# Kernel optimization log

Measured on AMD Instinct MI355X. Metric: run time of the kernel, lower is better.

## Reference

```python
import jax, jax.numpy as jnp
import numpy as np

N = 100_000      # nodes
E = 1_600_000    # edges (avg degree 16)
C_IN, C_H, C_OUT = 32, 64, 64
G = 64           # graphs in batch


def setup_inputs() -> dict:
    key = jax.random.key(0)
    ks = jax.random.split(key, 10)
    x = jax.random.normal(ks[0], (N, C_IN), jnp.float32)
    edge_index = jax.random.randint(ks[1], (2, E), 0, N, dtype=jnp.int64)
    edge_weight = jax.random.uniform(ks[2], (E,), jnp.float32)
    batch = jnp.sort(jax.random.randint(ks[3], (N,), 0, G, dtype=jnp.int64))
    def lin(k, fan_in, fan_out):
        return jax.random.normal(k, (fan_in, fan_out), jnp.float32) / np.float32(np.sqrt(fan_in))
    W1 = lin(ks[4], C_IN, C_H)
    W2 = lin(ks[5], C_H, C_H)
    W3 = lin(ks[6], C_H, C_OUT)
    b1 = jnp.zeros((C_H,), jnp.float32)
    b2 = jnp.zeros((C_H,), jnp.float32)
    b3 = jnp.zeros((C_OUT,), jnp.float32)
    return {"x": x, "edge_weight": edge_weight, "W1": W1, "b1": b1,
            "W2": W2, "b2": b2, "W3": W3, "b3": b3,
            "edge_index": edge_index, "batch": batch}


def _gcn_norm(edge_index, edge_weight, n):
    # PyG GCNConv default: add self-loops (weight 1), symmetric D^-1/2 A D^-1/2 norm.
    loop = jnp.arange(n, dtype=edge_index.dtype)
    src = jnp.concatenate([edge_index[0], loop])
    dst = jnp.concatenate([edge_index[1], loop])
    ew = jnp.concatenate([edge_weight, jnp.ones((n,), edge_weight.dtype)])
    deg = jax.ops.segment_sum(ew, dst, num_segments=n)
    dis = jnp.where(deg > 0, jax.lax.rsqrt(deg), jnp.float32(0))
    norm = dis[src] * ew * dis[dst]
    return src, dst, norm


def _gcn_layer(h, W, b, src, dst, norm, n):
    h = h @ W                                 # [N, out]
    msg = h[src] * norm[:, None]              # gather + scale  [E+N, out]
    agg = jax.ops.segment_sum(msg, dst, num_segments=n)
    return agg + b


def reference(x, edge_weight, W1, b1, W2, b2, W3, b3, edge_index, batch):
    n = x.shape[0]
    src, dst, norm = _gcn_norm(edge_index, edge_weight, n)  # shared across layers
    h = jax.nn.silu(_gcn_layer(x, W1, b1, src, dst, norm, n))
    # Dropout(0.1) is identity in eval mode
    h = jax.nn.silu(_gcn_layer(h, W2, b2, src, dst, norm, n))
    h = jax.nn.silu(_gcn_layer(h, W3, b3, src, dst, norm, n))
    # global_mean_pool over graphs
    sums = jax.ops.segment_sum(h, batch, num_segments=G)
    counts = jax.ops.segment_sum(jnp.ones((n,), h.dtype), batch, num_segments=G)
    return sums / jnp.maximum(counts, 1)[:, None]
```

## Files before the change

kernel.cpp:

```cpp
#include <hip/hip_runtime.h>
#include <hip/hip_fp16.h>
#include <math.h>


#define NB   256
#define PBLK 1024
#define FIXP_SCALE 1048576.0f
#define FIXP_MASK  ((1ULL << 40) - 1)

__device__ __forceinline__ int lower_bound_i(const int* __restrict__ a, int n, int v) {
    int lo = 0, hi = n;
    while (lo < hi) {
        int m = (lo + hi) >> 1;
        if (a[m] < v) lo = m + 1; else hi = m;
    }
    return lo;
}

__global__ __launch_bounds__(256) void k_bhist(const int* __restrict__ dst,
                                               int* __restrict__ hcnt, int e) {
    __shared__ int hist[NB];
    int tid = threadIdx.x, blk = blockIdx.x;
    hist[tid] = 0;
    __syncthreads();
    int chunk = (e + PBLK - 1) / PBLK;
    int lo = blk * chunk, hi = min(e, lo + chunk);
    for (int i = lo + tid; i < hi; i += 256)
        atomicAdd(&hist[dst[i] >> 9], 1);
    __syncthreads();
    hcnt[tid * PBLK + blk] = hist[tid];
}

__global__ __launch_bounds__(256) void k_bscan(int* __restrict__ hcnt,
                                               int* __restrict__ btot) {
    __shared__ int s[256];
    int b = blockIdx.x, tid = threadIdx.x;
    int* row = hcnt + b * PBLK;
    int a0 = row[4 * tid], a1 = row[4 * tid + 1], a2 = row[4 * tid + 2], a3 = row[4 * tid + 3];
    int tsum = a0 + a1 + a2 + a3;
    s[tid] = tsum;
    __syncthreads();
    for (int off = 1; off < 256; off <<= 1) {
        int t = (tid >= off) ? s[tid - off] : 0;
        __syncthreads();
        s[tid] += t;
        __syncthreads();
    }
    int ex = s[tid] - tsum;
    row[4 * tid] = ex;
    row[4 * tid + 1] = ex + a0;
    row[4 * tid + 2] = ex + a0 + a1;
    row[4 * tid + 3] = ex + a0 + a1 + a2;
    if (tid == 255) btot[b] = s[255];
}

__global__ __launch_bounds__(256) void k_bbase(const int* __restrict__ btot,
                                               int* __restrict__ bbase,
                                               int* __restrict__ rowptr, int n, int e) {
    __shared__ int s[256];
    int tid = threadIdx.x;
    int v = btot[tid];
    s[tid] = v;
    __syncthreads();
    for (int off = 1; off < 256; off <<= 1) {
        int t = (tid >= off) ? s[tid - off] : 0;
        __syncthreads();
        s[tid] += t;
        __syncthreads();
    }
    bbase[tid] = s[tid] - v;
    if (tid == 255) bbase[NB] = s[255];
    if (tid == 0) rowptr[n] = e;
}

__global__ __launch_bounds__(256) void k_bpart(const int* __restrict__ src,
                                               const int* __restrict__ dst,
                                               const float* __restrict__ ew,
                                               const int* __restrict__ hcnt,
                                               const int* __restrict__ bbase,
                                               int2* __restrict__ bedge, int e) {
    __shared__ int cur[NB];
    int tid = threadIdx.x, blk = blockIdx.x;
    cur[tid] = bbase[tid] + hcnt[tid * PBLK + blk];
    __syncthreads();
    int chunk = (e + PBLK - 1) / PBLK;
    int lo = blk * chunk, hi = min(e, lo + chunk);
    for (int i = lo + tid; i < hi; i += 256) {
        int d = dst[i];
        int pos = atomicAdd(&cur[d >> 9], 1);
        bedge[pos] = make_int2(src[i] | ((d & 511) << 17), __float_as_int(ew[i]));
    }
}

__global__ __launch_bounds__(256) void k_bucket(const int2* __restrict__ bedge,
                                                const int* __restrict__ bbase,
                                                float* __restrict__ dis,
                                                int* __restrict__ rowptr,
                                                int2* __restrict__ em, int n) {
    __shared__ unsigned long long pk[512];
    __shared__ int cnt[512];
    __shared__ int scn[512];
    __shared__ float sdis[512];
    __shared__ int cur[512];
    int b = blockIdx.x, tid = threadIdx.x;
    int e0 = bbase[b], e1 = bbase[b + 1];
    pk[tid] = 0ULL; pk[tid + 256] = 0ULL;
    __syncthreads();
    for (int i = e0 + tid; i < e1; i += 256) {
        int2 v = bedge[i];
        int dlo = (v.x >> 17) & 511;
        unsigned long long p =
            (1ULL << 40) | (unsigned long long)(__int_as_float(v.y) * FIXP_SCALE);
        atomicAdd(&pk[dlo], p);
    }
    __syncthreads();
#pragma unroll
    for (int k = 0; k < 2; ++k) {
        int i = tid + k * 256;
        unsigned long long v = pk[i];
        int c = (int)(v >> 40);
        cnt[i] = c; scn[i] = c;
        sdis[i] = rsqrtf(1.0f + (float)(v & FIXP_MASK) * (1.0f / FIXP_SCALE));
    }
    __syncthreads();
    for (int off = 1; off < 512; off <<= 1) {
        int i0 = tid, i1 = tid + 256;
        int v0 = (i0 >= off) ? scn[i0 - off] : 0;
        int v1 = (i1 >= off) ? scn[i1 - off] : 0;
        __syncthreads();
        scn[i0] += v0; scn[i1] += v1;
        __syncthreads();
    }
#pragma unroll
    for (int k = 0; k < 2; ++k) {
        int i = tid + k * 256;
        int rb = e0 + scn[i] - cnt[i];
        cur[i] = rb;
        int node = (b << 9) + i;
        if (node < n) { rowptr[node] = rb; dis[node] = sdis[i]; }
    }
    __syncthreads();
    for (int i = e0 + tid; i < e1; i += 256) {
        int2 v = bedge[i];
        int dlo = (v.x >> 17) & 511;
        int pos = atomicAdd(&cur[dlo], 1);
        float w = __int_as_float(v.y) * sdis[dlo];
        em[pos] = make_int2(v.x & 0x1FFFF, __float_as_int(w));
    }
}

__global__ void k_scale(const float* __restrict__ x, const float* __restrict__ dis,
                        __half* __restrict__ hs, int total) {
    int idx = blockIdx.x * blockDim.x + threadIdx.x;
    if (idx < total) hs[idx] = __float2half(x[idx] * dis[idx >> 5]);
}

__device__ __forceinline__ float2 cvt_pair(unsigned int u) {
    __half2 h2 = *(__half2*)&u;
    return __half22float2(h2);
}

__global__ __launch_bounds__(256, 4) void k_agg32(const __half* __restrict__ hs,
                                                  const int2* __restrict__ em,
                                                  const int* __restrict__ rowptr,
                                                  const float* __restrict__ dis,
                                                  __half* __restrict__ y0, int n) {
    __shared__ __align__(8) int2 sme[4][128];
    int lane = threadIdx.x & 63, wv = threadIdx.x >> 6;
    int c = lane & 15, quarter = lane >> 4;
    const unsigned int* h32 = (const unsigned int*)hs;
    int wid = (blockIdx.x * blockDim.x + threadIdx.x) >> 6;
    int n0 = wid * 8;
    if (n0 >= n) return;
    int cnt = min(8, n - n0);
    int rp = 0;
    if (lane <= cnt) rp = rowptr[n0 + lane];
    int hiw = __shfl(rp, cnt, 64);
    int wlo = 0, whi = 0;
    for (int k = 0; k < cnt; ++k) {
        int node = n0 + k;
        int lo = __shfl(rp, k, 64), hi = __shfl(rp, k + 1, 64);
        float2 acc = make_float2(0.0f, 0.0f);
        if (quarter == 0) {
            float di = dis[node];
            float2 hv = cvt_pair(h32[(unsigned)(node * 16 + c)]);
            acc.x = di * hv.x; acc.y = di * hv.y;
        }
        int idx = lo;
        while (idx < hi) {
            if (idx >= whi) {
                int i0 = idx + lane;
                if (i0 < hiw) sme[wv][lane] = em[i0];
                if (idx + 64 < hiw) {
                    int i1 = i0 + 64;
                    if (i1 < hiw) sme[wv][lane + 64] = em[i1];
                }
                wlo = idx; whi = idx + 128;
            }
            int base = idx - wlo;
            int take = min(hi, whi) - idx;
            for (int g = 0; g < take; g += 16) {
                int2 ev[4]; unsigned int hv[4]; int pr[4];
#pragma unroll
                for (int t = 0; t < 4; ++t) {
                    int p = g + 4 * t + quarter;
                    pr[t] = p < take;
                    int pc = pr[t] ? p : 0;
                    ev[t] = sme[wv][base + pc];
                }
#pragma unroll
                for (int t = 0; t < 4; ++t)
                    hv[t] = h32[(unsigned)(ev[t].x * 16 + c)];
#pragma unroll
                for (int t = 0; t < 4; ++t) {
                    float ww = pr[t] ? __int_as_float(ev[t].y) : 0.0f;
                    float2 hf = cvt_pair(hv[t]);
                    acc.x = fmaf(ww, hf.x, acc.x);
                    acc.y = fmaf(ww, hf.y, acc.y);
                }
            }
            idx += take;
        }
        acc.x += __shfl_down(acc.x, 32, 64);
        acc.y += __shfl_down(acc.y, 32, 64);
        acc.x += __shfl_down(acc.x, 16, 64);
        acc.y += __shfl_down(acc.y, 16, 64);
        if (quarter == 0)
            ((__half2*)y0)[(size_t)node * 16 + c] =
                __float22half2_rn(make_float2(acc.x, acc.y));
    }
}

__global__ __launch_bounds__(256, 2) void k_mm32act(const __half* __restrict__ y0,
                                                    const float* __restrict__ W,
                                                    const float* __restrict__ bias,
                                                    const float* __restrict__ dis,
                                                    __half* __restrict__ out, int n) {
    __shared__ __align__(16) float sw[32 * 64 + 64];
#pragma unroll
    for (int i = 0; i < 8; ++i)
        sw[threadIdx.x + 256 * i] = W[threadIdx.x + 256 * i];
    if (threadIdx.x < 64) sw[2048 + threadIdx.x] = bias[threadIdx.x];
    __syncthreads();
    int node = blockIdx.x * 256 + threadIdx.x;
    if (node >= n) return;
    uint4 yp[4];
    const uint4* yrow = (const uint4*)(y0 + (size_t)node * 32);
#pragma unroll
    for (int i = 0; i < 4; ++i) yp[i] = yrow[i];
    const unsigned int* ypk = (const unsigned int*)yp;
    float o[64];
#pragma unroll
    for (int j = 0; j < 64; ++j) o[j] = sw[2048 + j];
#pragma unroll
    for (int k2 = 0; k2 < 16; ++k2) {
        float2 yk = cvt_pair(ypk[k2]);
        const float4* r0 = (const float4*)&sw[(2 * k2) * 64];
        const float4* r1 = (const float4*)&sw[(2 * k2 + 1) * 64];
#pragma unroll
        for (int j4 = 0; j4 < 16; ++j4) {
            float4 w0 = r0[j4];
            float4 w1 = r1[j4];
            o[4 * j4 + 0] = fmaf(yk.y, w1.x, fmaf(yk.x, w0.x, o[4 * j4 + 0]));
            o[4 * j4 + 1] = fmaf(yk.y, w1.y, fmaf(yk.x, w0.y, o[4 * j4 + 1]));
            o[4 * j4 + 2] = fmaf(yk.y, w1.z, fmaf(yk.x, w0.z, o[4 * j4 + 2]));
            o[4 * j4 + 3] = fmaf(yk.y, w1.w, fmaf(yk.x, w0.w, o[4 * j4 + 3]));
        }
    }
    float dsc = dis[node];
    __half2* orow = (__half2*)(out + (size_t)node * 64);
#pragma unroll
    for (int j2 = 0; j2 < 32; ++j2) {
        float ox = o[2 * j2], oy = o[2 * j2 + 1];
        ox = ox / (1.0f + __expf(-ox)) * dsc;
        oy = oy / (1.0f + __expf(-oy)) * dsc;
        orow[j2] = __float22half2_rn(make_float2(ox, oy));
    }
}

__global__ __launch_bounds__(256, 2) void k_mm64(const __half* __restrict__ y,
                                                 const float* __restrict__ W,
                                                 __half* __restrict__ z, int n) {
    __shared__ __align__(16) float sw[64 * 64];
#pragma unroll
    for (int i = 0; i < 16; ++i)
        sw[threadIdx.x + 256 * i] = W[threadIdx.x + 256 * i];
    __syncthreads();
    int node = blockIdx.x * 256 + threadIdx.x;
    if (node >= n) return;
    uint4 yp[8];
    const uint4* yrow = (const uint4*)(y + (size_t)node * 64);
#pragma unroll
    for (int i = 0; i < 8; ++i) yp[i] = yrow[i];
    const unsigned int* ypk = (const unsigned int*)yp;
    float o[64];
#pragma unroll
    for (int j = 0; j < 64; ++j) o[j] = 0.0f;
#pragma unroll
    for (int k2 = 0; k2 < 32; ++k2) {
        float2 yk = cvt_pair(ypk[k2]);
        const float4* r0 = (const float4*)&sw[(2 * k2) * 64];
        const float4* r1 = (const float4*)&sw[(2 * k2 + 1) * 64];
#pragma unroll
        for (int j4 = 0; j4 < 16; ++j4) {
            float4 w0 = r0[j4];
            float4 w1 = r1[j4];
            o[4 * j4 + 0] = fmaf(yk.y, w1.x, fmaf(yk.x, w0.x, o[4 * j4 + 0]));
            o[4 * j4 + 1] = fmaf(yk.y, w1.y, fmaf(yk.x, w0.y, o[4 * j4 + 1]));
            o[4 * j4 + 2] = fmaf(yk.y, w1.z, fmaf(yk.x, w0.z, o[4 * j4 + 2]));
            o[4 * j4 + 3] = fmaf(yk.y, w1.w, fmaf(yk.x, w0.w, o[4 * j4 + 3]));
        }
    }
    __half2* zrow = (__half2*)(z + (size_t)node * 64);
#pragma unroll
    for (int j2 = 0; j2 < 32; ++j2)
        zrow[j2] = __float22half2_rn(make_float2(o[2 * j2], o[2 * j2 + 1]));
}

template <bool SCALE, typename OUT>
__global__ __launch_bounds__(256, 4) void k_agg64(const __half* __restrict__ z,
                                                  const int2* __restrict__ em,
                                                  const int* __restrict__ rowptr,
                                                  const float* __restrict__ dis,
                                                  const float* __restrict__ bias,
                                                  OUT* __restrict__ out, int n) {
    __shared__ __align__(8) int2 sme[4][128];
    int lane = threadIdx.x & 63, wv = threadIdx.x >> 6;
    int c = lane & 31, half = lane >> 5;
    const unsigned int* h32 = (const unsigned int*)z;
    float2 bv2 = ((const float2*)bias)[c];
    int wid = (blockIdx.x * blockDim.x + threadIdx.x) >> 6;
    int n0 = wid * 8;
    if (n0 >= n) return;
    int cnt = min(8, n - n0);
    int rp = 0;
    if (lane <= cnt) rp = rowptr[n0 + lane];
    int hiw = __shfl(rp, cnt, 64);
    int wlo = 0, whi = 0;
    for (int k = 0; k < cnt; ++k) {
        int node = n0 + k;
        int lo = __shfl(rp, k, 64), hi = __shfl(rp, k + 1, 64);
        float di = 0.0f;
        float2 acc = make_float2(0.0f, 0.0f);
        if (half == 0) {
            di = dis[node];
            float2 hv = cvt_pair(h32[(unsigned)(node * 32 + c)]);
            acc.x = di * hv.x; acc.y = di * hv.y;
        }
        int idx = lo;
        while (idx < hi) {
            if (idx >= whi) {
                int i0 = idx + lane;
                if (i0 < hiw) sme[wv][lane] = em[i0];
                if (idx + 64 < hiw) {
                    int i1 = i0 + 64;
                    if (i1 < hiw) sme[wv][lane + 64] = em[i1];
                }
                wlo = idx; whi = idx + 128;
            }
            int base = idx - wlo;
            int take = min(hi, whi) - idx;
            for (int g = 0; g < take; g += 16) {
                int2 ev[8]; unsigned int hv[8]; int pr[8];
#pragma unroll
                for (int t = 0; t < 8; ++t) {
                    int p = g + 2 * t + half;
                    pr[t] = p < take;
                    int pc = pr[t] ? p : 0;
                    ev[t] = sme[wv][base + pc];
                }
#pragma unroll
                for (int t = 0; t < 8; ++t)
                    hv[t] = h32[(unsigned)(ev[t].x * 32 + c)];
#pragma unroll
                for (int t = 0; t < 8; ++t) {
                    float ww = pr[t] ? __int_as_float(ev[t].y) : 0.0f;
                    float2 hf = cvt_pair(hv[t]);
                    acc.x = fmaf(ww, hf.x, acc.x);
                    acc.y = fmaf(ww, hf.y, acc.y);
                }
            }
            idx += take;
        }
        acc.x += __shfl_down(acc.x, 32, 64);
        acc.y += __shfl_down(acc.y, 32, 64);
        if (half == 0) {
            float ox = acc.x + bv2.x, oy = acc.y + bv2.y;
            ox = ox / (1.0f + __expf(-ox));
            oy = oy / (1.0f + __expf(-oy));
            if (SCALE) { ox *= di; oy *= di; }
            if (sizeof(OUT) == 2) {
                ((__half2*)out)[(size_t)node * 32 + c] =
                    __float22half2_rn(make_float2(ox, oy));
            } else {
                ((float2*)out)[(size_t)node * 32 + c] = make_float2(ox, oy);
            }
        }
    }
}

__global__ void k_pool_partial(const float* __restrict__ h, const int* __restrict__ batch,
                               float* __restrict__ acc, int n) {
    int c = threadIdx.x & 63, r = threadIdx.x >> 6;
    int base = blockIdx.x * 128;
    int end = base + 128; if (end > n) end = n;
    float part = 0.0f;
    int cur = -1;
    for (int i = base + r; i < end; i += 4) {
        int g = batch[i];
        if (g != cur) {
            if (cur >= 0) atomicAdd(&acc[cur * 64 + c], part);
            part = 0.0f;
            cur = g;
        }
        part += h[(size_t)i * 64 + c];
    }
    if (cur >= 0) atomicAdd(&acc[cur * 64 + c], part);
}

__global__ void k_pool_final(const float* __restrict__ acc, const int* __restrict__ batch,
                             float* __restrict__ out, int n) {
    int idx = blockIdx.x * blockDim.x + threadIdx.x;
    int g = idx >> 6;
    int lo = lower_bound_i(batch, n, g);
    int hi = lower_bound_i(batch, n, g + 1);
    int cnt = hi - lo;
    out[idx] = acc[idx] / (float)(cnt > 0 ? cnt : 1);
}

extern "C" void kernel_launch(void* const* d_in, const int* in_sizes, int n_in,
                              void* d_out, int out_size, void* d_ws, size_t ws_size,
                              hipStream_t stream) {
    const float* x   = (const float*)d_in[0];
    const float* ew  = (const float*)d_in[1];
    const float* W1  = (const float*)d_in[2];
    const float* b1  = (const float*)d_in[3];
    const float* W2  = (const float*)d_in[4];
    const float* b2  = (const float*)d_in[5];
    const float* W3  = (const float*)d_in[6];
    const float* b3  = (const float*)d_in[7];
    const int*   eidx  = (const int*)d_in[8];
    const int*   batch = (const int*)d_in[9];
    float* out = (float*)d_out;

    const int E = in_sizes[1];
    const int N = in_sizes[9];
    const int G = 64;
    const int* src = eidx;
    const int* dst = eidx + E;

    char* p = (char*)d_ws;
    __half* A     = (__half*)p;                p += (size_t)N * 64 * sizeof(__half);
    __half* B     = (__half*)p;                p += (size_t)N * 64 * sizeof(__half);
    float* C      = (float*)p;                 p += (size_t)N * 64 * sizeof(float);
    float* dis    = (float*)p;                 p += (size_t)N * sizeof(float);
    int*   rowptr = (int*)p;                   p += (size_t)(N + 1) * sizeof(int);
    int*   bbase  = (int*)p;                   p += (size_t)(NB + 1) * sizeof(int);
    float* acc    = (float*)p;                 p += (size_t)G * 64 * sizeof(float);
    p = (char*)(((uintptr_t)p + 7) & ~(uintptr_t)7);
    int2*  em     = (int2*)p;

    int2* bedge = (int2*)A;
    int*  hcnt  = (int*)B;
    int*  btot  = (int*)B + NB * PBLK;

    const int BT = 256;
    const int WAVES = (N + 7) / 8;
    const int AGG_BLOCKS = (WAVES + 3) / 4;
    const int MM_BLOCKS = (N + 255) / 256;

    k_bhist<<<PBLK, 256, 0, stream>>>(dst, hcnt, E);
    k_bscan<<<NB, 256, 0, stream>>>(hcnt, btot);
    k_bbase<<<1, 256, 0, stream>>>(btot, bbase, rowptr, N, E);
    k_bpart<<<PBLK, 256, 0, stream>>>(src, dst, ew, hcnt, bbase, bedge, E);
    k_bucket<<<NB, 256, 0, stream>>>(bedge, bbase, dis, rowptr, em, N);

    k_scale<<<(N * 32 + BT - 1) / BT, BT, 0, stream>>>(x, dis, (__half*)B, N * 32);
    k_agg32<<<AGG_BLOCKS, BT, 0, stream>>>((__half*)B, em, rowptr, dis, (__half*)C, N);
    k_mm32act<<<MM_BLOCKS, BT, 0, stream>>>((__half*)C, W1, b1, dis, A, N);

    k_mm64<<<MM_BLOCKS, BT, 0, stream>>>(A, W2, B, N);
    k_agg64<true, __half><<<AGG_BLOCKS, BT, 0, stream>>>(B, em, rowptr, dis, b2, A, N);

    k_mm64<<<MM_BLOCKS, BT, 0, stream>>>(A, W3, B, N);
    k_agg64<false, float><<<AGG_BLOCKS, BT, 0, stream>>>(B, em, rowptr, dis, b3, C, N);

    hipMemsetAsync(acc, 0, (size_t)G * 64 * sizeof(float), stream);
    k_pool_partial<<<(N + 127) / 128, BT, 0, stream>>>(C, batch, acc, N);
    k_pool_final<<<(G * 64) / BT, BT, 0, stream>>>(acc, batch, out, N);
}
```

Before: 364.6 us.

## Fuse scaling into bucket kernel, merge layer1 and layer2 matmuls, widen aggregation loads

Folds the x*dis fp16 conversion into the bucket kernel, removing a separate launch and a re-read of dis. Fuses the first-layer matmul and activation with the second-layer matmul into one kernel, so the intermediate activation never goes to global memory. Widens the gather in both aggregation kernels to 8-byte loads per lane, so each lane processes four channels and more edges run in parallel per wave. The fused matmul holds 64 accumulators plus 32 temporaries per thread, which raises register pressure (launch bounds 256,1) and may lower occupancy.

Measured after the change: 369.0 us. Within noise of the previous version (+1.2%).

```diff
diff --git a/kernel.cpp b/kernel.cpp
--- a/kernel.cpp
+++ b/kernel.cpp
@@ -96,7 +96,9 @@
                                                 const int* __restrict__ bbase,
                                                 float* __restrict__ dis,
                                                 int* __restrict__ rowptr,
-                                                int2* __restrict__ em, int n) {
+                                                int2* __restrict__ em,
+                                                const float* __restrict__ x,
+                                                __half* __restrict__ hs, int n) {
     __shared__ unsigned long long pk[512];
     __shared__ int cnt[512];
     __shared__ int scn[512];
@@ -147,12 +149,18 @@
         float w = __int_as_float(v.y) * sdis[dlo];
         em[pos] = make_int2(v.x & 0x1FFFF, __float_as_int(w));
     }
-}
-
-__global__ void k_scale(const float* __restrict__ x, const float* __restrict__ dis,
-                        __half* __restrict__ hs, int total) {
-    int idx = blockIdx.x * blockDim.x + threadIdx.x;
-    if (idx < total) hs[idx] = __float2half(x[idx] * dis[idx >> 5]);
+    int nodebase = b << 9;
+    int nloc = n - nodebase; if (nloc > 512) nloc = 512;
+    if (nloc > 0) {
+        const float2* x2 = (const float2*)(x + (size_t)nodebase * 32);
+        __half2* hs2 = (__half2*)(hs + (size_t)nodebase * 32);
+        int total2 = nloc * 16;
+        for (int i = tid; i < total2; i += 256) {
+            float d = sdis[i >> 4];
+            float2 v = x2[i];
+            hs2[i] = __float22half2_rn(make_float2(v.x * d, v.y * d));
+        }
+    }
 }
 
 __device__ __forceinline__ float2 cvt_pair(unsigned int u) {
@@ -167,8 +175,8 @@
                                                   __half* __restrict__ y0, int n) {
     __shared__ __align__(8) int2 sme[4][128];
     int lane = threadIdx.x & 63, wv = threadIdx.x >> 6;
-    int c = lane & 15, quarter = lane >> 4;
-    const unsigned int* h32 = (const unsigned int*)hs;
+    int c = lane & 7, oct = lane >> 3;
+    const uint2* h64 = (const uint2*)hs;
     int wid = (blockIdx.x * blockDim.x + threadIdx.x) >> 6;
     int n0 = wid * 8;
     if (n0 >= n) return;
@@ -180,67 +188,79 @@
     for (int k = 0; k < cnt; ++k) {
         int node = n0 + k;
         int lo = __shfl(rp, k, 64), hi = __shfl(rp, k + 1, 64);
-        float2 acc = make_float2(0.0f, 0.0f);
-        if (quarter == 0) {
+        float2 a0 = make_float2(0.0f, 0.0f), a1 = make_float2(0.0f, 0.0f);
+        if (oct == 0) {
             float di = dis[node];
-            float2 hv = cvt_pair(h32[(unsigned)(node * 16 + c)]);
-            acc.x = di * hv.x; acc.y = di * hv.y;
+            uint2 sh = h64[(unsigned)(node * 8 + c)];
+            float2 f0 = cvt_pair(sh.x), f1 = cvt_pair(sh.y);
+            a0.x = di * f0.x; a0.y = di * f0.y;
+            a1.x = di * f1.x; a1.y = di * f1.y;
         }
         int idx = lo;
         while (idx < hi) {
             if (idx >= whi) {
                 int i0 = idx + lane;
                 if (i0 < hiw) sme[wv][lane] = em[i0];
-                if (idx + 64 < hiw) {
-                    int i1 = i0 + 64;
-                    if (i1 < hiw) sme[wv][lane + 64] = em[i1];
-                }
+                int i1 = i0 + 64;
+                if (i1 < hiw) sme[wv][lane + 64] = em[i1];
                 wlo = idx; whi = idx + 128;
             }
             int base = idx - wlo;
             int take = min(hi, whi) - idx;
-            for (int g = 0; g < take; g += 16) {
-                int2 ev[4]; unsigned int hv[4]; int pr[4];
+            for (int g = 0; g < take; g += 32) {
+                int2 ev[4]; uint2 hv[4]; int pr[4];
 #pragma unroll
                 for (int t = 0; t < 4; ++t) {
-                    int p = g + 4 * t + quarter;
+                    int p = g + 8 * t + oct;
                     pr[t] = p < take;
                     int pc = pr[t] ? p : 0;
                     ev[t] = sme[wv][base + pc];
                 }
 #pragma unroll
                 for (int t = 0; t < 4; ++t)
-                    hv[t] = h32[(unsigned)(ev[t].x * 16 + c)];
+                    hv[t] = h64[(unsigned)(ev[t].x * 8 + c)];
 #pragma unroll
                 for (int t = 0; t < 4; ++t) {
                     float ww = pr[t] ? __int_as_float(ev[t].y) : 0.0f;
-                    float2 hf = cvt_pair(hv[t]);
-                    acc.x = fmaf(ww, hf.x, acc.x);
-                    acc.y = fmaf(ww, hf.y, acc.y);
+                    float2 f0 = cvt_pair(hv[t].x), f1 = cvt_pair(hv[t].y);
+                    a0.x = fmaf(ww, f0.x, a0.x);
+                    a0.y = fmaf(ww, f0.y, a0.y);
+                    a1.x = fmaf(ww, f1.x, a1.x);
+                    a1.y = fmaf(ww, f1.y, a1.y);
                 }
             }
             idx += take;
         }
-        acc.x += __shfl_down(acc.x, 32, 64);
-        acc.y += __shfl_down(acc.y, 32, 64);
-        acc.x += __shfl_down(acc.x, 16, 64);
-        acc.y += __shfl_down(acc.y, 16, 64);
-        if (quarter == 0)
-            ((__half2*)y0)[(size_t)node * 16 + c] =
-                __float22half2_rn(make_float2(acc.x, acc.y));
-    }
-}
-
-__global__ __launch_bounds__(256, 2) void k_mm32act(const __half* __restrict__ y0,
-                                                    const float* __restrict__ W,
-                                                    const float* __restrict__ bias,
-                                                    const float* __restrict__ dis,
-                                                    __half* __restrict__ out, int n) {
-    __shared__ __align__(16) float sw[32 * 64 + 64];
-#pragma unroll
-    for (int i = 0; i < 8; ++i)
-        sw[threadIdx.x + 256 * i] = W[threadIdx.x + 256 * i];
-    if (threadIdx.x < 64) sw[2048 + threadIdx.x] = bias[threadIdx.x];
+        a0.x += __shfl_down(a0.x, 32, 64); a0.y += __shfl_down(a0.y, 32, 64);
+        a1.x += __shfl_down(a1.x, 32, 64); a1.y += __shfl_down(a1.y, 32, 64);
+        a0.x += __shfl_down(a0.x, 16, 64); a0.y += __shfl_down(a0.y, 16, 64);
+        a1.x += __shfl_down(a1.x, 16, 64); a1.y += __shfl_down(a1.y, 16, 64);
+        a0.x += __shfl_down(a0.x, 8, 64);  a0.y += __shfl_down(a0.y, 8, 64);
+        a1.x += __shfl_down(a1.x, 8, 64);  a1.y += __shfl_down(a1.y, 8, 64);
+        if (oct == 0) {
+            uint2 o;
+            __half2 p0 = __float22half2_rn(make_float2(a0.x, a0.y));
+            __half2 p1 = __float22half2_rn(make_float2(a1.x, a1.y));
+            o.x = *(unsigned int*)&p0; o.y = *(unsigned int*)&p1;
+            ((uint2*)y0)[(size_t)node * 8 + c] = o;
+        }
+    }
+}
+
+__global__ __launch_bounds__(256, 1) void k_mmf12(const __half* __restrict__ y0,
+                                                  const float* __restrict__ W1,
+                                                  const float* __restrict__ b1,
+                                                  const float* __restrict__ W2,
+                                                  const float* __restrict__ dis,
+                                                  __half* __restrict__ z2, int n) {
+    __shared__ __align__(16) float sw1[32 * 64];
+    __shared__ __align__(16) float sw2[64 * 64];
+    __shared__ float sb[64];
+#pragma unroll
+    for (int i = 0; i < 8; ++i) sw1[threadIdx.x + 256 * i] = W1[threadIdx.x + 256 * i];
+#pragma unroll
+    for (int i = 0; i < 16; ++i) sw2[threadIdx.x + 256 * i] = W2[threadIdx.x + 256 * i];
+    if (threadIdx.x < 64) sb[threadIdx.x] = b1[threadIdx.x];
     __syncthreads();
     int node = blockIdx.x * 256 + threadIdx.x;
     if (node >= n) return;
@@ -251,12 +271,12 @@
     const unsigned int* ypk = (const unsigned int*)yp;
     float o[64];
 #pragma unroll
-    for (int j = 0; j < 64; ++j) o[j] = sw[2048 + j];
+    for (int j = 0; j < 64; ++j) o[j] = sb[j];
 #pragma unroll
     for (int k2 = 0; k2 < 16; ++k2) {
         float2 yk = cvt_pair(ypk[k2]);
-        const float4* r0 = (const float4*)&sw[(2 * k2) * 64];
-        const float4* r1 = (const float4*)&sw[(2 * k2 + 1) * 64];
+        const float4* r0 = (const float4*)&sw1[(2 * k2) * 64];
+        const float4* r1 = (const float4*)&sw1[(2 * k2 + 1) * 64];
 #pragma unroll
         for (int j4 = 0; j4 < 16; ++j4) {
             float4 w0 = r0[j4];
@@ -268,13 +288,34 @@
         }
     }
     float dsc = dis[node];
-    __half2* orow = (__half2*)(out + (size_t)node * 64);
-#pragma unroll
-    for (int j2 = 0; j2 < 32; ++j2) {
-        float ox = o[2 * j2], oy = o[2 * j2 + 1];
-        ox = ox / (1.0f + __expf(-ox)) * dsc;
-        oy = oy / (1.0f + __expf(-oy)) * dsc;
-        orow[j2] = __float22half2_rn(make_float2(ox, oy));
+#pragma unroll
+    for (int j = 0; j < 64; ++j) {
+        float v = o[j];
+        o[j] = v / (1.0f + __expf(-v)) * dsc;
+    }
+    __half2* zrow = (__half2*)(z2 + (size_t)node * 64);
+#pragma unroll
+    for (int hblk = 0; hblk < 2; ++hblk) {
+        float z[32];
+#pragma unroll
+        for (int j = 0; j < 32; ++j) z[j] = 0.0f;
+#pragma unroll
+        for (int k = 0; k < 64; ++k) {
+            float a = o[k];
+            const float4* r = (const float4*)&sw2[k * 64 + hblk * 32];
+#pragma unroll
+            for (int j4 = 0; j4 < 8; ++j4) {
+                float4 w = r[j4];
+                z[4 * j4 + 0] = fmaf(a, w.x, z[4 * j4 + 0]);
+                z[4 * j4 + 1] = fmaf(a, w.y, z[4 * j4 + 1]);
+                z[4 * j4 + 2] = fmaf(a, w.z, z[4 * j4 + 2]);
+                z[4 * j4 + 3] = fmaf(a, w.w, z[4 * j4 + 3]);
+            }
+        }
+#pragma unroll
+        for (int j2 = 0; j2 < 16; ++j2)
+            zrow[hblk * 16 + j2] =
+                __float22half2_rn(make_float2(z[2 * j2], z[2 * j2 + 1]));
     }
 }
 
@@ -326,9 +367,9 @@
                                                   OUT* __restrict__ out, int n) {
     __shared__ __align__(8) int2 sme[4][128];
     int lane = threadIdx.x & 63, wv = threadIdx.x >> 6;
-    int c = lane & 31, half = lane >> 5;
-    const unsigned int* h32 = (const unsigned int*)z;
-    float2 bv2 = ((const float2*)bias)[c];
+    int c = lane & 15, quarter = lane >> 4;
+    const uint2* h64 = (const uint2*)z;
+    float4 bv4 = ((const float4*)bias)[c];
     int wid = (blockIdx.x * blockDim.x + threadIdx.x) >> 6;
     int n0 = wid * 8;
     if (n0 >= n) return;
@@ -341,59 +382,69 @@
         int node = n0 + k;
         int lo = __shfl(rp, k, 64), hi = __shfl(rp, k + 1, 64);
         float di = 0.0f;
-        float2 acc = make_float2(0.0f, 0.0f);
-        if (half == 0) {
+        float2 a0 = make_float2(0.0f, 0.0f), a1 = make_float2(0.0f, 0.0f);
+        if (quarter == 0) {
             di = dis[node];
-            float2 hv = cvt_pair(h32[(unsigned)(node * 32 + c)]);
-            acc.x = di * hv.x; acc.y = di * hv.y;
+            uint2 sh = h64[(unsigned)(node * 16 + c)];
+            float2 f0 = cvt_pair(sh.x), f1 = cvt_pair(sh.y);
+            a0.x = di * f0.x; a0.y = di * f0.y;
+            a1.x = di * f1.x; a1.y = di * f1.y;
         }
         int idx = lo;
         while (idx < hi) {
             if (idx >= whi) {
                 int i0 = idx + lane;
                 if (i0 < hiw) sme[wv][lane] = em[i0];
-                if (idx + 64 < hiw) {
-                    int i1 = i0 + 64;
-                    if (i1 < hiw) sme[wv][lane + 64] = em[i1];
-                }
+                int i1 = i0 + 64;
+                if (i1 < hiw) sme[wv][lane + 64] = em[i1];
                 wlo = idx; whi = idx + 128;
             }
             int base = idx - wlo;
             int take = min(hi, whi) - idx;
             for (int g = 0; g < take; g += 16) {
-                int2 ev[8]; unsigned int hv[8]; int pr[8];
-#pragma unroll
-                for (int t = 0; t < 8; ++t) {
-                    int p = g + 2 * t + half;
+                int2 ev[4]; uint2 hv[4]; int pr[4];
+#pragma unroll
+                for (int t = 0; t < 4; ++t) {
+                    int p = g + 4 * t + quarter;
                     pr[t] = p < take;
                     int pc = pr[t] ? p : 0;
                     ev[t] = sme[wv][base + pc];
                 }
 #pragma unroll
-                for (int t = 0; t < 8; ++t)
-                    hv[t] = h32[(unsigned)(ev[t].x * 32 + c)];
-#pragma unroll
-                for (int t = 0; t < 8; ++t) {
+                for (int t = 0; t < 4; ++t)
+                    hv[t] = h64[(unsigned)(ev[t].x * 16 + c)];
+#pragma unroll
+                for (int t = 0; t < 4; ++t) {
                     float ww = pr[t] ? __int_as_float(ev[t].y) : 0.0f;
-                    float2 hf = cvt_pair(hv[t]);
-                    acc.x = fmaf(ww, hf.x, acc.x);
-                    acc.y = fmaf(ww, hf.y, acc.y);
+                    float2 f0 = cvt_pair(hv[t].x), f1 = cvt_pair(hv[t].y);
+                    a0.x = fmaf(ww, f0.x, a0.x);
+                    a0.y = fmaf(ww, f0.y, a0.y);
+                    a1.x = fmaf(ww, f1.x, a1.x);
+                    a1.y = fmaf(ww, f1.y, a1.y);
                 }
             }
             idx += take;
         }
-        acc.x += __shfl_down(acc.x, 32, 64);
-        acc.y += __shfl_down(acc.y, 32, 64);
-        if (half == 0) {
-            float ox = acc.x + bv2.x, oy = acc.y + bv2.y;
+        a0.x += __shfl_down(a0.x, 32, 64); a0.y += __shfl_down(a0.y, 32, 64);
+        a1.x += __shfl_down(a1.x, 32, 64); a1.y += __shfl_down(a1.y, 32, 64);
+        a0.x += __shfl_down(a0.x, 16, 64); a0.y += __shfl_down(a0.y, 16, 64);
+        a1.x += __shfl_down(a1.x, 16, 64); a1.y += __shfl_down(a1.y, 16, 64);
+        if (quarter == 0) {
+            float ox = a0.x + bv4.x, oy = a0.y + bv4.y;
+            float oz = a1.x + bv4.z, ow = a1.y + bv4.w;
             ox = ox / (1.0f + __expf(-ox));
             oy = oy / (1.0f + __expf(-oy));
-            if (SCALE) { ox *= di; oy *= di; }
+            oz = oz / (1.0f + __expf(-oz));
+            ow = ow / (1.0f + __expf(-ow));
+            if (SCALE) { ox *= di; oy *= di; oz *= di; ow *= di; }
             if (sizeof(OUT) == 2) {
-                ((__half2*)out)[(size_t)node * 32 + c] =
-                    __float22half2_rn(make_float2(ox, oy));
+                uint2 o;
+                __half2 p0 = __float22half2_rn(make_float2(ox, oy));
+                __half2 p1 = __float22half2_rn(make_float2(oz, ow));
+                o.x = *(unsigned int*)&p0; o.y = *(unsigned int*)&p1;
+                ((uint2*)out)[(size_t)node * 16 + c] = o;
             } else {
-                ((float2*)out)[(size_t)node * 32 + c] = make_float2(ox, oy);
+                ((float4*)out)[(size_t)node * 16 + c] = make_float4(ox, oy, oz, ow);
             }
         }
     }
@@ -473,13 +524,12 @@
     k_bscan<<<NB, 256, 0, stream>>>(hcnt, btot);
     k_bbase<<<1, 256, 0, stream>>>(btot, bbase, rowptr, N, E);
     k_bpart<<<PBLK, 256, 0, stream>>>(src, dst, ew, hcnt, bbase, bedge, E);
-    k_bucket<<<NB, 256, 0, stream>>>(bedge, bbase, dis, rowptr, em, N);
-
-    k_scale<<<(N * 32 + BT - 1) / BT, BT, 0, stream>>>(x, dis, (__half*)B, N * 32);
+    k_bucket<<<NB, 256, 0, stream>>>(bedge, bbase, dis, rowptr, em, x, (__half*)B, N);
+
     k_agg32<<<AGG_BLOCKS, BT, 0, stream>>>((__half*)B, em, rowptr, dis, (__half*)C, N);
-    k_mm32act<<<MM_BLOCKS, BT, 0, stream>>>((__half*)C, W1, b1, dis, A, N);
-
-    k_mm64<<<MM_BLOCKS, BT, 0, stream>>>(A, W2, B, N);
+
+    k_mmf12<<<MM_BLOCKS, BT, 0, stream>>>((__half*)C, W1, b1, W2, dis, (__half*)B, N);
+
     k_agg64<true, __half><<<AGG_BLOCKS, BT, 0, stream>>>(B, em, rowptr, dis, b2, A, N);
 
     k_mm64<<<MM_BLOCKS, BT, 0, stream>>>(A, W3, B, N);
```
